# Performance work log

Measured on AMD Instinct MI355X. Metric: run time of the kernel, lower is better.

The kernel has to match this reference:

```python
import jax, jax.numpy as jnp
import numpy as np


def setup_inputs() -> dict:
    key = jax.random.key(0)
    k1, k2, k3 = jax.random.split(key, 3)
    B, T, C = 4, 2048, 1024
    x = jax.random.normal(k1, (B, T, C), dtype=jnp.float32)
    w_attn = jax.random.normal(k2, (C, 3 * C), dtype=jnp.float32) * 0.02
    b_attn = jnp.zeros((3 * C,), dtype=jnp.float32)
    w_proj = jax.random.normal(k3, (C, C), dtype=jnp.float32) * 0.02
    b_proj = jnp.zeros((C,), dtype=jnp.float32)
    return {"x": x, "w_attn": w_attn, "b_attn": b_attn, "w_proj": w_proj, "b_proj": b_proj}


def reference(x, w_attn, b_attn, w_proj, b_proj):
    B, T, C = x.shape
    n_head = 16
    head_size = C // n_head
    qkv = x @ w_attn + b_attn                      # [B, T, 3C]
    q, k, v = jnp.split(qkv, 3, axis=-1)
    # [B, H, T, Dh]
    q = q.reshape(B, T, n_head, head_size).transpose(0, 2, 1, 3)
    k = k.reshape(B, T, n_head, head_size).transpose(0, 2, 1, 3)
    v = v.reshape(B, T, n_head, head_size).transpose(0, 2, 1, 3)
    scale = 1.0 / jnp.sqrt(jnp.float32(head_size))
    att = jnp.einsum("bhqd,bhkd->bhqk", q, k) * scale   # [B, H, T, T]
    causal = jnp.tril(jnp.ones((T, T), dtype=bool))
    att = jnp.where(causal[None, None], att, jnp.float32(-jnp.inf))
    att = jax.nn.softmax(att, axis=-1)
    y = jnp.einsum("bhqk,bhkd->bhqd", att, v)            # [B, H, T, Dh]
    y = y.transpose(0, 2, 1, 3).reshape(B, T, C)
    return y @ w_proj + b_proj
```

## Files before the change

kernel.cpp:

```cpp
#include <hip/hip_runtime.h>
#include <hip/hip_bf16.h>
#include <math.h>


typedef __attribute__((ext_vector_type(8))) short short8;
typedef __attribute__((ext_vector_type(4))) float f32x4;

__device__ __forceinline__ short f2bf(float f) {
    __hip_bfloat16 h = __float2bfloat16(f);
    return *reinterpret_cast<short*>(&h);
}
__device__ __forceinline__ float bf2f(short s) {
    __hip_bfloat16 h = *reinterpret_cast<__hip_bfloat16*>(&s);
    return __bfloat162float(h);
}

#define MFMA16(a, b, c) __builtin_amdgcn_mfma_f32_16x16x32_bf16((a), (b), (c), 0, 0, 0)

__device__ __forceinline__ void gload_lds16(const short* g, short* l) {
    __builtin_amdgcn_global_load_lds(
        (const __attribute__((address_space(1))) void*)g,
        (__attribute__((address_space(3))) void*)l, 16, 0, 0);
}

__global__ void sniff_kernel(const unsigned int* __restrict__ xb,
                             unsigned int* __restrict__ flag)
{
    __shared__ int cnt;
    if (threadIdx.x == 0) cnt = 0;
    __syncthreads();
    int c = 0;
    for (int i = threadIdx.x; i < 4096; i += 256) {
        unsigned e = (xb[i] >> 7) & 0xFFu;
        if (e >= 96u && e <= 142u) ++c;
    }
    atomicAdd(&cnt, c);
    __syncthreads();
    if (threadIdx.x == 0) *flag = (cnt < 2048) ? 1u : 0u;
}

__global__ __launch_bounds__(256)
void cvt_x(const void* __restrict__ in, short* __restrict__ out,
           const unsigned int* __restrict__ flagp)
{
    const bool f32in = (*flagp != 0u);
    const size_t i = ((size_t)blockIdx.x * 256 + threadIdx.x) * 8;
    if (f32in) {
        const float* f = (const float*)in + i;
        f32x4 u0 = *(const f32x4*)f;
        f32x4 u1 = *(const f32x4*)(f + 4);
        short8 v;
#pragma unroll
        for (int j = 0; j < 4; ++j) { v[j] = f2bf(u0[j]); v[j + 4] = f2bf(u1[j]); }
        *(short8*)(out + i) = v;
    } else {
        *(short8*)(out + i) = *(const short8*)((const short*)in + i);
    }
}

__global__ __launch_bounds__(256)
void transpose_cvt(const void* __restrict__ in, short* __restrict__ out,
                   int R, int C, const unsigned int* __restrict__ flagp)
{
    const bool f32in = (*flagp != 0u);
    __shared__ short tile[64][65];
    const int bx = blockIdx.x * 64;
    const int by = blockIdx.y * 64;
    const int tx = threadIdx.x & 63;
    const int ty = threadIdx.x >> 6;
#pragma unroll
    for (int i = 0; i < 64; i += 4) {
        size_t idx = (size_t)(by + ty + i) * C + bx + tx;
        tile[ty + i][tx] = f32in ? f2bf(((const float*)in)[idx])
                                 : ((const short*)in)[idx];
    }
    __syncthreads();
#pragma unroll
    for (int i = 0; i < 64; i += 4)
        out[(size_t)(bx + ty + i) * R + by + tx] = tile[tx][ty + i];
}

template <int EPI>
__global__ __launch_bounds__(256)
void gemm_kernel(const short* __restrict__ A,
                 const short* __restrict__ Bt,
                 const void* __restrict__ bias,
                 void* __restrict__ O0,
                 short* __restrict__ O1,
                 short* __restrict__ O2,
                 int M, int N, int K,
                 const unsigned int* __restrict__ flagp)
{
    const bool f32io = (*flagp != 0u);
    __shared__ __align__(16) short ldsA[3 * 128 * 32];
    __shared__ __align__(16) short ldsB[3 * 128 * 32];

    const int tid = threadIdx.x;
    const int lane = tid & 63;
    const int wv = tid >> 6;
    const int wm = (wv & 1) * 64;
    const int wn = (wv >> 1) * 64;
    const int tile_m = blockIdx.y * 128;
    const int tile_n = blockIdx.x * 128;

    f32x4 acc[4][4];
#pragma unroll
    for (int i = 0; i < 4; ++i)
#pragma unroll
        for (int j = 0; j < 4; ++j) acc[i][j] = (f32x4){0.f, 0.f, 0.f, 0.f};

    const int ar = lane & 15;
    const int aq = (lane >> 4) * 8;
    const int lrow = lane >> 2;
    const int lcol = (lane & 3) << 3;

    auto stage = [&](int k0, int bsel) {
#pragma unroll
        for (int p = 0; p < 2; ++p) {
            int c = wv * 2 + p;
            int row = c * 16 + lrow;
            gload_lds16(A + (size_t)(tile_m + row) * K + k0 + lcol,
                        ldsA + bsel * 4096 + c * 512);
            gload_lds16(Bt + (size_t)(tile_n + row) * K + k0 + lcol,
                        ldsB + bsel * 4096 + c * 512);
        }
    };

    stage(0, 0);
    stage(32, 1);
    int cur = 0;

    for (int k0 = 0; k0 < K; k0 += 32) {
        if (k0 + 32 < K) {
            asm volatile("s_waitcnt vmcnt(4)\n\ts_barrier" ::: "memory");
        } else {
            asm volatile("s_waitcnt vmcnt(0)\n\ts_barrier" ::: "memory");
        }

        int nb = cur + 2; if (nb >= 3) nb -= 3;
        if (k0 + 64 < K) stage(k0 + 64, nb);

        const short* Ab = ldsA + cur * 4096;
        const short* Bb = ldsB + cur * 4096;
        short8 af[4], bfr[4];
#pragma unroll
        for (int i = 0; i < 4; ++i)
            af[i] = *(const short8*)(Ab + (wm + i * 16 + ar) * 32 + aq);
#pragma unroll
        for (int j = 0; j < 4; ++j)
            bfr[j] = *(const short8*)(Bb + (wn + j * 16 + ar) * 32 + aq);
#pragma unroll
        for (int i = 0; i < 4; ++i)
#pragma unroll
            for (int j = 0; j < 4; ++j)
                acc[i][j] = MFMA16(af[i], bfr[j], acc[i][j]);

        ++cur; if (cur == 3) cur = 0;
    }

    const int colq = lane & 15;
    const int rowq = (lane >> 4) * 4;
#pragma unroll
    for (int j = 0; j < 4; ++j) {
        int gn = tile_n + wn + j * 16 + colq;
        float bv = f32io ? ((const float*)bias)[gn] : bf2f(((const short*)bias)[gn]);
#pragma unroll
        for (int i = 0; i < 4; ++i) {
#pragma unroll
            for (int r = 0; r < 4; ++r) {
                int gm = tile_m + wm + i * 16 + rowq + r;
                float val = acc[i][j][r] + bv;
                if (EPI == 0) {
                    if (f32io) ((float*)O0)[(size_t)gm * N + gn] = val;
                    else       ((short*)O0)[(size_t)gm * N + gn] = f2bf(val);
                } else {
                    int which = gn >> 10;
                    int c = gn & 1023;
                    int h = c >> 6;
                    int d = c & 63;
                    int b = gm >> 11;
                    int t = gm & 2047;
                    size_t bh = (size_t)(b * 16 + h);
                    short o = f2bf(which == 0 ? val * 0.18033688011112042f : val);
                    if (which == 0)      ((short*)O0)[(bh * 2048 + t) * 64 + d] = o;
                    else if (which == 1) O1[(bh * 2048 + t) * 64 + d] = o;
                    else                 O2[(bh * 64 + d) * 2048 + t] = o;
                }
            }
        }
    }
}

__global__ __launch_bounds__(256, 4)
void attn_kernel(const short* __restrict__ Q,
                 const short* __restrict__ Kp_,
                 const short* __restrict__ Vt,
                 short* __restrict__ Y)
{
    __shared__ __align__(16) short ldsK[2 * 64 * 64];
    __shared__ __align__(16) short ldsV[2 * 64 * 64];
    __shared__ __align__(16) short pbuf[4][16 * 64];

    const int tid = threadIdx.x;
    const int lane = tid & 63;
    const int wv = tid >> 6;
    const int m16 = lane & 15;
    const int quad = lane >> 4;

    const int fid = blockIdx.x;
    const int xcd = fid & 7;
    const int slot = fid >> 3;
    const int bh = (xcd << 3) | (slot >> 4);
    const int g = slot & 15;

    const int b = bh >> 4, h = bh & 15;

    const short* Qp = Q   + (size_t)bh * 2048 * 64;
    const short* Kp = Kp_ + (size_t)bh * 2048 * 64;
    const short* Vp = Vt  + (size_t)bh * 64 * 2048;
    short* pw = pbuf[wv];

    const int srow = lane >> 3;
    const int sw = (((lane & 7) ^ (srow & 7)) << 3);
    const int swr = ((m16 & 7) << 3);
    const int pswr = swr;

    auto stage = [&](int kb, int bsel) {
#pragma unroll
        for (int p = 0; p < 2; ++p) {
            const int c8 = wv * 2 + p;
            const int row = c8 * 8 + srow;
            gload_lds16(Kp + (size_t)(kb + row) * 64 + sw,
                        ldsK + bsel * 4096 + c8 * 512);
            gload_lds16(Vp + (size_t)row * 2048 + kb + sw,
                        ldsV + bsel * 4096 + c8 * 512);
        }
    };

#pragma unroll
    for (int pass = 0; pass < 2; ++pass) {
        const int t = pass ? (31 - g) : g;
        const int qbase = t * 64 + wv * 16;

        stage(0, 0);

        short8 aq0 = *(const short8*)(Qp + (size_t)(qbase + m16) * 64 + quad * 8);
        short8 aq1 = *(const short8*)(Qp + (size_t)(qbase + m16) * 64 + 32 + quad * 8);

        __syncthreads();
        int cur = 0;

        f32x4 o[4];
#pragma unroll
        for (int dt = 0; dt < 4; ++dt) o[dt] = (f32x4){0.f, 0.f, 0.f, 0.f};
        float lrow[4] = {0.f, 0.f, 0.f, 0.f};

        for (int kt = 0; kt <= t; ++kt) {
            const int kb = kt << 6;
            if (kt < t) stage(kb + 64, cur ^ 1);

            const short* kbase = ldsK + cur * 4096;
            const short* vbase = ldsV + cur * 4096;

            f32x4 s[4];
            __builtin_amdgcn_s_setprio(1);
#pragma unroll
            for (int c = 0; c < 4; ++c) {
                const short* kr = kbase + (c * 16 + m16) * 64;
                short8 kf0 = *(const short8*)(kr + ((quad * 8) ^ swr));
                short8 kf1 = *(const short8*)(kr + ((quad * 8 + 32) ^ swr));
                f32x4 z = (f32x4){0.f, 0.f, 0.f, 0.f};
                z = MFMA16(aq0, kf0, z);
                z = MFMA16(aq1, kf1, z);
                s[c] = z;
            }
            __builtin_amdgcn_s_setprio(0);

            if (kt < t) {
#pragma unroll
                for (int c = 0; c < 4; ++c) {
#pragma unroll
                    for (int r = 0; r < 4; ++r) {
                        const int qrow = quad * 4 + r;
                        float p = exp2f(s[c][r]);
                        lrow[r] += p;
                        pw[qrow * 64 + ((c * 16 + m16) ^ ((qrow & 7) << 3))] = f2bf(p);
                    }
                }
            } else {
#pragma unroll
                for (int c = 0; c < 4; ++c) {
                    const int key = kb + c * 16 + m16;
                    const bool needmask = (kb + c * 16 + 15 > qbase);
#pragma unroll
                    for (int r = 0; r < 4; ++r) {
                        const int qrow = quad * 4 + r;
                        float p = exp2f(s[c][r]);
                        if (needmask && key > qbase + qrow) p = 0.f;
                        lrow[r] += p;
                        pw[qrow * 64 + ((c * 16 + m16) ^ ((qrow & 7) << 3))] = f2bf(p);
                    }
                }
            }

            asm volatile("" ::: "memory");
            short8 ap0 = *(const short8*)(pw + m16 * 64 + ((quad * 8) ^ pswr));
            short8 ap1 = *(const short8*)(pw + m16 * 64 + ((quad * 8 + 32) ^ pswr));
            asm volatile("" ::: "memory");

            __builtin_amdgcn_s_setprio(1);
#pragma unroll
            for (int dt = 0; dt < 4; ++dt) {
                const short* vr = vbase + (dt * 16 + m16) * 64;
                short8 vf0 = *(const short8*)(vr + ((quad * 8) ^ swr));
                short8 vf1 = *(const short8*)(vr + ((quad * 8 + 32) ^ swr));
                o[dt] = MFMA16(ap0, vf0, o[dt]);
                o[dt] = MFMA16(ap1, vf1, o[dt]);
            }
            __builtin_amdgcn_s_setprio(0);

            __syncthreads();
            cur ^= 1;
        }

        float linv[4];
#pragma unroll
        for (int r = 0; r < 4; ++r) {
            float sm = lrow[r];
#pragma unroll
            for (int off = 1; off < 16; off <<= 1)
                sm += __shfl_xor(sm, off);
            linv[r] = 1.0f / sm;
        }
#pragma unroll
        for (int dt = 0; dt < 4; ++dt) {
#pragma unroll
            for (int r = 0; r < 4; ++r) {
                int row = qbase + quad * 4 + r;
                int col = h * 64 + dt * 16 + m16;
                Y[((size_t)(b * 2048 + row)) * 1024 + col] = f2bf(o[dt][r] * linv[r]);
            }
        }
    }
}

extern "C" void kernel_launch(void* const* d_in, const int* in_sizes, int n_in,
                              void* d_out, int out_size, void* d_ws, size_t ws_size,
                              hipStream_t stream)
{
    const void* x      = d_in[0];
    const void* w_attn = d_in[1];
    const void* b_attn = d_in[2];
    const void* w_proj = d_in[3];
    const void* b_proj = d_in[4];

    char* ws = (char*)d_ws;
    unsigned int* flag = (unsigned int*)(ws + 0);
    short* Wta = (short*)(ws + 256);
    short* Wtp = (short*)(ws + 6291712);
    short* Qb  = (short*)(ws + 8388864);
    short* Kb  = (short*)(ws + 25166080);
    short* Vtb = (short*)(ws + 41943296);
    short* Yb  = (short*)(ws + 58720512);
    short* Xb  = (short*)(ws + 58720512);

    sniff_kernel<<<1, 256, 0, stream>>>((const unsigned int*)x, flag);
    cvt_x<<<dim3(4096), 256, 0, stream>>>(x, Xb, flag);
    transpose_cvt<<<dim3(48, 16), 256, 0, stream>>>(w_attn, Wta, 1024, 3072, flag);
    transpose_cvt<<<dim3(16, 16), 256, 0, stream>>>(w_proj, Wtp, 1024, 1024, flag);
    gemm_kernel<1><<<dim3(24, 64), 256, 0, stream>>>(Xb, Wta, b_attn, Qb, Kb, Vtb,
                                                     8192, 3072, 1024, flag);
    attn_kernel<<<dim3(1024), 256, 0, stream>>>(Qb, Kb, Vtb, Yb);
    gemm_kernel<0><<<dim3(8, 64), 256, 0, stream>>>(Yb, Wtp, b_proj, d_out, nullptr, nullptr,
                                                    8192, 1024, 1024, flag);
}
```

Measured before the change: 325.5 us.

## Merge prep kernels, swizzle GEMM tiles per XCD, single-buffer attention with one tile per block

Folds the x conversion and both weight transposes into one launch, cutting two kernel launches. Remaps GEMM block indices so that each XCD works on a contiguous band of N tiles, aiming for better L2 reuse. The attention kernel now handles one query tile per block (2048 blocks, longest first) instead of a balanced pair of tiles. It also drops K/V double-buffering to halve LDS use and raises the occupancy target to 6. The risk is that K/V loads are no longer overlapped with compute, since each iteration now waits on its own stage.

```diff
diff --git a/kernel.cpp b/kernel.cpp
--- a/kernel.cpp
+++ b/kernel.cpp
@@ -40,32 +40,39 @@
 }
 
 __global__ __launch_bounds__(256)
-void cvt_x(const void* __restrict__ in, short* __restrict__ out,
-           const unsigned int* __restrict__ flagp)
+void prep_kernel(const void* __restrict__ x, short* __restrict__ Xb,
+                 const void* __restrict__ w_attn, short* __restrict__ Wta,
+                 const void* __restrict__ w_proj, short* __restrict__ Wtp,
+                 const unsigned int* __restrict__ flagp)
 {
     const bool f32in = (*flagp != 0u);
-    const size_t i = ((size_t)blockIdx.x * 256 + threadIdx.x) * 8;
-    if (f32in) {
-        const float* f = (const float*)in + i;
-        f32x4 u0 = *(const f32x4*)f;
-        f32x4 u1 = *(const f32x4*)(f + 4);
-        short8 v;
-#pragma unroll
-        for (int j = 0; j < 4; ++j) { v[j] = f2bf(u0[j]); v[j + 4] = f2bf(u1[j]); }
-        *(short8*)(out + i) = v;
+    const int bid = blockIdx.x;
+    if (bid < 4096) {
+        const size_t i = ((size_t)bid * 256 + threadIdx.x) * 8;
+        if (f32in) {
+            const float* f = (const float*)x + i;
+            f32x4 u0 = *(const f32x4*)f;
+            f32x4 u1 = *(const f32x4*)(f + 4);
+            short8 v;
+#pragma unroll
+            for (int j = 0; j < 4; ++j) { v[j] = f2bf(u0[j]); v[j + 4] = f2bf(u1[j]); }
+            *(short8*)(Xb + i) = v;
+        } else {
+            *(short8*)(Xb + i) = *(const short8*)((const short*)x + i);
+        }
+        return;
+    }
+    __shared__ short tile[64][65];
+    const void* in; short* out; int R, C, bx, by;
+    if (bid < 4864) {
+        const int b2 = bid - 4096;
+        in = w_attn; out = Wta; R = 1024; C = 3072;
+        bx = (b2 % 48) * 64; by = (b2 / 48) * 64;
     } else {
-        *(short8*)(out + i) = *(const short8*)((const short*)in + i);
-    }
-}
-
-__global__ __launch_bounds__(256)
-void transpose_cvt(const void* __restrict__ in, short* __restrict__ out,
-                   int R, int C, const unsigned int* __restrict__ flagp)
-{
-    const bool f32in = (*flagp != 0u);
-    __shared__ short tile[64][65];
-    const int bx = blockIdx.x * 64;
-    const int by = blockIdx.y * 64;
+        const int b2 = bid - 4864;
+        in = w_proj; out = Wtp; R = 1024; C = 1024;
+        bx = (b2 % 16) * 64; by = (b2 / 16) * 64;
+    }
     const int tx = threadIdx.x & 63;
     const int ty = threadIdx.x >> 6;
 #pragma unroll
@@ -100,8 +107,14 @@
     const int wv = tid >> 6;
     const int wm = (wv & 1) * 64;
     const int wn = (wv >> 1) * 64;
-    const int tile_m = blockIdx.y * 128;
-    const int tile_n = blockIdx.x * 128;
+
+    const int gx = gridDim.x;
+    const int lin = blockIdx.y * gx + blockIdx.x;
+    const int cpx = gx >> 3;
+    const int xcd = lin & 7;
+    const int rest = lin >> 3;
+    const int tile_n = (xcd * cpx + (rest % cpx)) * 128;
+    const int tile_m = (rest / cpx) * 128;
 
     f32x4 acc[4][4];
 #pragma unroll
@@ -191,14 +204,14 @@
     }
 }
 
-__global__ __launch_bounds__(256, 4)
+__global__ __launch_bounds__(256, 6)
 void attn_kernel(const short* __restrict__ Q,
                  const short* __restrict__ Kp_,
                  const short* __restrict__ Vt,
                  short* __restrict__ Y)
 {
-    __shared__ __align__(16) short ldsK[2 * 64 * 64];
-    __shared__ __align__(16) short ldsV[2 * 64 * 64];
+    __shared__ __align__(16) short ldsK[64 * 64];
+    __shared__ __align__(16) short ldsV[64 * 64];
     __shared__ __align__(16) short pbuf[4][16 * 64];
 
     const int tid = threadIdx.x;
@@ -210,10 +223,12 @@
     const int fid = blockIdx.x;
     const int xcd = fid & 7;
     const int slot = fid >> 3;
-    const int bh = (xcd << 3) | (slot >> 4);
-    const int g = slot & 15;
+    const int bh = (xcd << 3) | (slot >> 5);
+    const int sub = slot & 31;
+    const int t = 31 - sub;
 
     const int b = bh >> 4, h = bh & 15;
+    const int qbase = t * 64 + wv * 16;
 
     const short* Qp = Q   + (size_t)bh * 2048 * 64;
     const short* Kp = Kp_ + (size_t)bh * 2048 * 64;
@@ -225,121 +240,105 @@
     const int swr = ((m16 & 7) << 3);
     const int pswr = swr;
 
-    auto stage = [&](int kb, int bsel) {
+    auto stage = [&](int kb) {
 #pragma unroll
         for (int p = 0; p < 2; ++p) {
             const int c8 = wv * 2 + p;
             const int row = c8 * 8 + srow;
-            gload_lds16(Kp + (size_t)(kb + row) * 64 + sw,
-                        ldsK + bsel * 4096 + c8 * 512);
-            gload_lds16(Vp + (size_t)row * 2048 + kb + sw,
-                        ldsV + bsel * 4096 + c8 * 512);
+            gload_lds16(Kp + (size_t)(kb + row) * 64 + sw, ldsK + c8 * 512);
+            gload_lds16(Vp + (size_t)row * 2048 + kb + sw, ldsV + c8 * 512);
         }
     };
 
-#pragma unroll
-    for (int pass = 0; pass < 2; ++pass) {
-        const int t = pass ? (31 - g) : g;
-        const int qbase = t * 64 + wv * 16;
-
-        stage(0, 0);
-
-        short8 aq0 = *(const short8*)(Qp + (size_t)(qbase + m16) * 64 + quad * 8);
-        short8 aq1 = *(const short8*)(Qp + (size_t)(qbase + m16) * 64 + 32 + quad * 8);
-
+    short8 aq0 = *(const short8*)(Qp + (size_t)(qbase + m16) * 64 + quad * 8);
+    short8 aq1 = *(const short8*)(Qp + (size_t)(qbase + m16) * 64 + 32 + quad * 8);
+
+    f32x4 o[4];
+#pragma unroll
+    for (int dt = 0; dt < 4; ++dt) o[dt] = (f32x4){0.f, 0.f, 0.f, 0.f};
+    float lrow[4] = {0.f, 0.f, 0.f, 0.f};
+
+    for (int kt = 0; kt <= t; ++kt) {
+        const int kb = kt << 6;
+        stage(kb);
         __syncthreads();
-        int cur = 0;
-
-        f32x4 o[4];
-#pragma unroll
-        for (int dt = 0; dt < 4; ++dt) o[dt] = (f32x4){0.f, 0.f, 0.f, 0.f};
-        float lrow[4] = {0.f, 0.f, 0.f, 0.f};
-
-        for (int kt = 0; kt <= t; ++kt) {
-            const int kb = kt << 6;
-            if (kt < t) stage(kb + 64, cur ^ 1);
-
-            const short* kbase = ldsK + cur * 4096;
-            const short* vbase = ldsV + cur * 4096;
-
-            f32x4 s[4];
-            __builtin_amdgcn_s_setprio(1);
+
+        f32x4 s[4];
+        __builtin_amdgcn_s_setprio(1);
+#pragma unroll
+        for (int c = 0; c < 4; ++c) {
+            const short* kr = ldsK + (c * 16 + m16) * 64;
+            short8 kf0 = *(const short8*)(kr + ((quad * 8) ^ swr));
+            short8 kf1 = *(const short8*)(kr + ((quad * 8 + 32) ^ swr));
+            f32x4 z = (f32x4){0.f, 0.f, 0.f, 0.f};
+            z = MFMA16(aq0, kf0, z);
+            z = MFMA16(aq1, kf1, z);
+            s[c] = z;
+        }
+        __builtin_amdgcn_s_setprio(0);
+
+        if (kt < t) {
 #pragma unroll
             for (int c = 0; c < 4; ++c) {
-                const short* kr = kbase + (c * 16 + m16) * 64;
-                short8 kf0 = *(const short8*)(kr + ((quad * 8) ^ swr));
-                short8 kf1 = *(const short8*)(kr + ((quad * 8 + 32) ^ swr));
-                f32x4 z = (f32x4){0.f, 0.f, 0.f, 0.f};
-                z = MFMA16(aq0, kf0, z);
-                z = MFMA16(aq1, kf1, z);
-                s[c] = z;
-            }
-            __builtin_amdgcn_s_setprio(0);
-
-            if (kt < t) {
-#pragma unroll
-                for (int c = 0; c < 4; ++c) {
-#pragma unroll
-                    for (int r = 0; r < 4; ++r) {
-                        const int qrow = quad * 4 + r;
-                        float p = exp2f(s[c][r]);
-                        lrow[r] += p;
-                        pw[qrow * 64 + ((c * 16 + m16) ^ ((qrow & 7) << 3))] = f2bf(p);
-                    }
-                }
-            } else {
-#pragma unroll
-                for (int c = 0; c < 4; ++c) {
-                    const int key = kb + c * 16 + m16;
-                    const bool needmask = (kb + c * 16 + 15 > qbase);
-#pragma unroll
-                    for (int r = 0; r < 4; ++r) {
-                        const int qrow = quad * 4 + r;
-                        float p = exp2f(s[c][r]);
-                        if (needmask && key > qbase + qrow) p = 0.f;
-                        lrow[r] += p;
-                        pw[qrow * 64 + ((c * 16 + m16) ^ ((qrow & 7) << 3))] = f2bf(p);
-                    }
+#pragma unroll
+                for (int r = 0; r < 4; ++r) {
+                    const int qrow = quad * 4 + r;
+                    float p = exp2f(s[c][r]);
+                    lrow[r] += p;
+                    pw[qrow * 64 + ((c * 16 + m16) ^ ((qrow & 7) << 3))] = f2bf(p);
                 }
             }
-
-            asm volatile("" ::: "memory");
-            short8 ap0 = *(const short8*)(pw + m16 * 64 + ((quad * 8) ^ pswr));
-            short8 ap1 = *(const short8*)(pw + m16 * 64 + ((quad * 8 + 32) ^ pswr));
-            asm volatile("" ::: "memory");
-
-            __builtin_amdgcn_s_setprio(1);
-#pragma unroll
-            for (int dt = 0; dt < 4; ++dt) {
-                const short* vr = vbase + (dt * 16 + m16) * 64;
-                short8 vf0 = *(const short8*)(vr + ((quad * 8) ^ swr));
-                short8 vf1 = *(const short8*)(vr + ((quad * 8 + 32) ^ swr));
-                o[dt] = MFMA16(ap0, vf0, o[dt]);
-                o[dt] = MFMA16(ap1, vf1, o[dt]);
+        } else {
+#pragma unroll
+            for (int c = 0; c < 4; ++c) {
+                const int key = kb + c * 16 + m16;
+                const bool needmask = (kb + c * 16 + 15 > qbase);
+#pragma unroll
+                for (int r = 0; r < 4; ++r) {
+                    const int qrow = quad * 4 + r;
+                    float p = exp2f(s[c][r]);
+                    if (needmask && key > qbase + qrow) p = 0.f;
+                    lrow[r] += p;
+                    pw[qrow * 64 + ((c * 16 + m16) ^ ((qrow & 7) << 3))] = f2bf(p);
+                }
             }
-            __builtin_amdgcn_s_setprio(0);
-
-            __syncthreads();
-            cur ^= 1;
-        }
-
-        float linv[4];
+        }
+
+        asm volatile("" ::: "memory");
+        short8 ap0 = *(const short8*)(pw + m16 * 64 + ((quad * 8) ^ pswr));
+        short8 ap1 = *(const short8*)(pw + m16 * 64 + ((quad * 8 + 32) ^ pswr));
+        asm volatile("" ::: "memory");
+
+        __builtin_amdgcn_s_setprio(1);
+#pragma unroll
+        for (int dt = 0; dt < 4; ++dt) {
+            const short* vr = ldsV + (dt * 16 + m16) * 64;
+            short8 vf0 = *(const short8*)(vr + ((quad * 8) ^ swr));
+            short8 vf1 = *(const short8*)(vr + ((quad * 8 + 32) ^ swr));
+            o[dt] = MFMA16(ap0, vf0, o[dt]);
+            o[dt] = MFMA16(ap1, vf1, o[dt]);
+        }
+        __builtin_amdgcn_s_setprio(0);
+
+        if (kt < t) __syncthreads();
+    }
+
+    float linv[4];
+#pragma unroll
+    for (int r = 0; r < 4; ++r) {
+        float sm = lrow[r];
+#pragma unroll
+        for (int off = 1; off < 16; off <<= 1)
+            sm += __shfl_xor(sm, off);
+        linv[r] = 1.0f / sm;
+    }
+#pragma unroll
+    for (int dt = 0; dt < 4; ++dt) {
 #pragma unroll
         for (int r = 0; r < 4; ++r) {
-            float sm = lrow[r];
-#pragma unroll
-            for (int off = 1; off < 16; off <<= 1)
-                sm += __shfl_xor(sm, off);
-            linv[r] = 1.0f / sm;
-        }
-#pragma unroll
-        for (int dt = 0; dt < 4; ++dt) {
-#pragma unroll
-            for (int r = 0; r < 4; ++r) {
-                int row = qbase + quad * 4 + r;
-                int col = h * 64 + dt * 16 + m16;
-                Y[((size_t)(b * 2048 + row)) * 1024 + col] = f2bf(o[dt][r] * linv[r]);
-            }
+            int row = qbase + quad * 4 + r;
+            int col = h * 64 + dt * 16 + m16;
+            Y[((size_t)(b * 2048 + row)) * 1024 + col] = f2bf(o[dt][r] * linv[r]);
         }
     }
 }
@@ -365,12 +364,10 @@
     short* Xb  = (short*)(ws + 58720512);
 
     sniff_kernel<<<1, 256, 0, stream>>>((const unsigned int*)x, flag);
-    cvt_x<<<dim3(4096), 256, 0, stream>>>(x, Xb, flag);
-    transpose_cvt<<<dim3(48, 16), 256, 0, stream>>>(w_attn, Wta, 1024, 3072, flag);
-    transpose_cvt<<<dim3(16, 16), 256, 0, stream>>>(w_proj, Wtp, 1024, 1024, flag);
+    prep_kernel<<<dim3(5120), 256, 0, stream>>>(x, Xb, w_attn, Wta, w_proj, Wtp, flag);
     gemm_kernel<1><<<dim3(24, 64), 256, 0, stream>>>(Xb, Wta, b_attn, Qb, Kb, Vtb,
                                                      8192, 3072, 1024, flag);
-    attn_kernel<<<dim3(1024), 256, 0, stream>>>(Qb, Kb, Vtb, Yb);
+    attn_kernel<<<dim3(2048), 256, 0, stream>>>(Qb, Kb, Vtb, Yb);
     gemm_kernel<0><<<dim3(8, 64), 256, 0, stream>>>(Yb, Wtp, b_proj, d_out, nullptr, nullptr,
                                                     8192, 1024, 1024, flag);
 }
```

Result: slower. 572.6 us (+75.9%).
